# Kernel tuning notes

Hardware: AMD Instinct MI355X
Metric: run time of the kernel (lower is better)

Reference implementation:

```python
import jax, jax.numpy as jnp
import numpy as np

B, N, DI, DS, DP, DM, S = 64, 4096, 64, 64, 64, 128, 7
NUM_ITER = 3
EPS_ATTN = 1e-8
LN_EPS = 1e-5


def setup_inputs() -> dict:
    key = jax.random.key(0)
    ks = jax.random.split(key, 12)
    rn = lambda k, shp, sc=1.0: (jax.random.normal(k, shp, jnp.float32) * sc)
    return {
        "x": rn(ks[0], (B, N, DI)),
        "ln_inp_g": jnp.ones((DI,), jnp.float32),
        "ln_inp_b": jnp.zeros((DI,), jnp.float32),
        "ln_slot_g": jnp.ones((DS,), jnp.float32),
        "ln_slot_b": jnp.zeros((DS,), jnp.float32),
        "slots_init": rn(ks[1], (1, S, DS)),
        "Wk": rn(ks[2], (DI, DP), 1.0 / np.sqrt(DI)),
        "Wv": rn(ks[3], (DI, DP), 1.0 / np.sqrt(DI)),
        "Wq": rn(ks[4], (DS, DP), 1.0 / np.sqrt(DS)),
        "gru_wih": rn(ks[5], (3 * DS, DP), 1.0 / np.sqrt(DS)),
        "gru_whh": rn(ks[6], (3 * DS, DS), 1.0 / np.sqrt(DS)),
        "gru_bih": jnp.zeros((3 * DS,), jnp.float32),
        "gru_bhh": jnp.zeros((3 * DS,), jnp.float32),
        "mlp_w1": rn(ks[7], (DS, DM), 1.0 / np.sqrt(DS)),
        "mlp_b1": jnp.zeros((DM,), jnp.float32),
        "mlp_w2": rn(ks[8], (DM, DS), 1.0 / np.sqrt(DM)),
        "mlp_b2": jnp.zeros((DS,), jnp.float32),
    }


def _layernorm(x, g, b):
    m = jnp.mean(x, axis=-1, keepdims=True)
    v = jnp.mean(jnp.square(x - m), axis=-1, keepdims=True)
    return (x - m) * jax.lax.rsqrt(v + LN_EPS) * g + b


def _gru_cell(u, h, wih, whh, bih, bhh):
    # PyTorch GRUCell semantics
    gi = u @ wih.T + bih  # [*, 3*DS]
    gh = h @ whh.T + bhh
    ir, iz, inn = jnp.split(gi, 3, axis=-1)
    hr, hz, hn = jnp.split(gh, 3, axis=-1)
    r = jax.nn.sigmoid(ir + hr)
    z = jax.nn.sigmoid(iz + hz)
    n = jnp.tanh(inn + r * hn)
    return (1.0 - z) * n + z * h


def reference(x, ln_inp_g, ln_inp_b, ln_slot_g, ln_slot_b, slots_init,
              Wk, Wv, Wq, gru_wih, gru_whh, gru_bih, gru_bhh,
              mlp_w1, mlp_b1, mlp_w2, mlp_b2):
    x = _layernorm(x, ln_inp_g, ln_inp_b)          # [B,N,DI]
    k = x @ Wk                                      # [B,N,DP] (hoisted; x fixed across iters)
    v = x @ Wv                                      # [B,N,DP]
    slots = jnp.broadcast_to(slots_init, (x.shape[0], S, DS))
    scale = 1.0 / np.sqrt(DP)
    for _ in range(NUM_ITER):
        slots_prev = slots
        sn = _layernorm(slots, ln_slot_g, ln_slot_b)
        q = sn @ Wq                                 # [B,S,DP]
        attn = jnp.einsum('bnd,bsd->bns', k, q) * scale
        attn = jax.nn.softmax(attn, axis=-1) + EPS_ATTN      # softmax over slots
        weights = attn / jnp.sum(attn, axis=1, keepdims=True)  # normalize over N
        updates = jnp.einsum('bns,bnd->bsd', weights, v)     # [B,S,DP]
        h = _gru_cell(updates.reshape(-1, DP), slots_prev.reshape(-1, DS),
                      gru_wih, gru_whh, gru_bih, gru_bhh)
        slots = h.reshape(-1, S, DS)
        slots = slots + (jax.nn.relu(slots @ mlp_w1 + mlp_b1) @ mlp_w2 + mlp_b2)
    return slots
```

## Files before the change

### kernel.cpp

```cpp
#include <hip/hip_runtime.h>
#include <stdint.h>

#define L2E 1.44269504088896f

static __device__ __forceinline__ float wsum(float v) {
    #pragma unroll
    for (int m = 1; m < 64; m <<= 1) v += __shfl_xor(v, m, 64);
    return v;
}
static __device__ __forceinline__ float sigm(float x) {
    return 1.0f / (1.0f + __builtin_amdgcn_exp2f(-x * L2E));
}
static __device__ __forceinline__ float tanh_(float x) {
    const float ax = fabsf(x);
    const float t = __builtin_amdgcn_exp2f(-2.0f * ax * L2E);
    const float r = (1.0f - t) / (1.0f + t);
    return (x < 0.f) ? -r : r;
}

template <int CTRL>
static __device__ __forceinline__ float dppterm(float v) {
    return __int_as_float(__builtin_amdgcn_update_dpp(
        0, __float_as_int(v), CTRL, 0xF, 0xF, true));
}
static __device__ __forceinline__ float red8(float v) {
    v += dppterm<0xB1>(v);
    v += dppterm<0x4E>(v);
    v += dppterm<0x141>(v);
    return v;
}

__global__ __launch_bounds__(256) void init_kernel(
    const float* __restrict__ s0,
    const float* __restrict__ lsg, const float* __restrict__ lsb,
    const float* __restrict__ Wq,  const float* __restrict__ Wk,
    const float* __restrict__ lig, const float* __restrict__ lib,
    const float* __restrict__ wih, const float* __restrict__ whh,
    float* __restrict__ slots, float* __restrict__ gkq, float* __restrict__ aux,
    float* __restrict__ wihT, float* __restrict__ whhT, float* __restrict__ WkT)
{
    __shared__ float wkT[4096];
    __shared__ float scr[4][64];
    const int tid = threadIdx.x, lane = tid & 63, wv = tid >> 6;
    const int idx = blockIdx.x * 256 + tid;

    if (idx < 12288) {
        const int i = idx / 192, j = idx - i * 192;
        wihT[idx] = wih[j * 64 + i];
    } else if (idx < 24576) {
        const int o = idx - 12288;
        const int i = o / 192, j = o - i * 192;
        whhT[o] = whh[j * 64 + i];
    } else {
        const int o = idx - 24576;
        const int p = o >> 6, d = o & 63;
        WkT[o] = Wk[d * 64 + p];
    }

    const int r = blockIdx.x * 4 + wv;
    const int s = r % 7;
    #pragma unroll
    for (int i = tid; i < 4096; i += 256) {
        const int d = i >> 6, p = i & 63;
        wkT[p * 64 + d] = Wk[i];
    }
    const float h = s0[s * 64 + lane];
    slots[r * 64 + lane] = h;
    __syncthreads();

    const float mean = wsum(h) * (1.0f / 64.0f);
    const float d = h - mean;
    const float var = wsum(d * d) * (1.0f / 64.0f);
    const float rs = rsqrtf(var + 1e-5f);
    const float sn = d * rs * lsg[lane] + lsb[lane];
    scr[wv][lane] = sn;
    __syncthreads();
    float q = 0.f;
    #pragma unroll 8
    for (int i = 0; i < 64; ++i) q = fmaf(scr[wv][i], Wq[i * 64 + lane], q);
    q *= 0.125f;
    __syncthreads();
    scr[wv][lane] = q;
    __syncthreads();
    float kq = 0.f;
    #pragma unroll 8
    for (int p = 0; p < 64; ++p) kq = fmaf(wkT[p * 64 + lane], scr[wv][p], kq);
    const float bk = wsum(lib[lane] * kq);
    const float gk = lig[lane] * kq;
    const float g1 = wsum(gk);
    gkq[r * 64 + lane] = gk;
    if (lane == 0) { aux[r * 2] = g1; aux[r * 2 + 1] = bk; }
}

__global__ __launch_bounds__(256, 2) void attn_kernel(
    const float* __restrict__ x,
    const float* __restrict__ gkq, const float* __restrict__ aux,
    float* __restrict__ Ypart)
{
    __shared__ float ybuf[16][460];
    const int tid = threadIdx.x, lane = tid & 63, wv = tid >> 6;
    const int b = blockIdx.x >> 4, chunk16 = blockIdx.x & 15;
    const int ck  = lane & 7;
    const int rsl = lane >> 3;

    float gk[7][8];
    {
        const float4* gp = (const float4*)(gkq + b * 448 + ck * 8);
        #pragma unroll
        for (int s = 0; s < 7; ++s) {
            const float4 u0 = gp[s * 16], u1 = gp[s * 16 + 1];
            gk[s][0] = u0.x; gk[s][1] = u0.y; gk[s][2] = u0.z; gk[s][3] = u0.w;
            gk[s][4] = u1.x; gk[s][5] = u1.y; gk[s][6] = u1.z; gk[s][7] = u1.w;
        }
    }
    const float* ab = aux + b * 14;
    float g1[7], bk[7];
    #pragma unroll
    for (int s = 0; s < 7; ++s) { g1[s] = ab[2 * s]; bk[s] = ab[2 * s + 1]; }

    float Yacc[7][8];
    #pragma unroll
    for (int s = 0; s < 7; ++s)
        #pragma unroll
        for (int j = 0; j < 8; ++j) Yacc[s][j] = 0.f;
    float cacc[7] = {0.f, 0.f, 0.f, 0.f, 0.f, 0.f, 0.f};

    const float* rb = x + (((long)b * 4096) + chunk16 * 256 + wv * 64 + rsl) * 64
                        + ck * 8;
    float4 a0 = *(const float4*)(rb);
    float4 a1 = *(const float4*)(rb + 4);
    #pragma unroll 1
    for (int g = 0; g < 8; ++g) {
        const int gn = (g < 7) ? g + 1 : 7;
        const float4 b0 = *(const float4*)(rb + gn * 512);
        const float4 b1 = *(const float4*)(rb + gn * 512 + 4);

        const float xv[8] = {a0.x, a0.y, a0.z, a0.w, a1.x, a1.y, a1.z, a1.w};
        float sum = 0.f, ss = 0.f;
        #pragma unroll
        for (int j = 0; j < 8; ++j) { sum += xv[j]; ss = fmaf(xv[j], xv[j], ss); }
        float acc[7];
        #pragma unroll
        for (int s = 0; s < 7; ++s) {
            float a = 0.f;
            #pragma unroll
            for (int j = 0; j < 8; ++j) a = fmaf(xv[j], gk[s][j], a);
            acc[s] = a;
        }
        sum = red8(sum);
        ss  = red8(ss);
        #pragma unroll
        for (int s = 0; s < 7; ++s) acc[s] = red8(acc[s]);

        const float m   = sum * (1.0f / 64.0f);
        const float var = ss * (1.0f / 64.0f) - m * m;
        const float rs  = rsqrtf(var + 1e-5f);
        const float rsm = rs * m;
        float t[7];
        #pragma unroll
        for (int s = 0; s < 7; ++s)
            t[s] = fmaf(rs, acc[s], fmaf(-rsm, g1[s], bk[s]));
        float mx = t[0];
        #pragma unroll
        for (int s = 1; s < 7; ++s) mx = fmaxf(mx, t[s]);
        float e[7], se = 0.f;
        #pragma unroll
        for (int s = 0; s < 7; ++s) {
            e[s] = __builtin_amdgcn_exp2f((t[s] - mx) * L2E);
            se += e[s];
        }
        const float inv = 1.0f / se;
        #pragma unroll
        for (int s = 0; s < 7; ++s) {
            const float w = fmaf(e[s], inv, 1e-8f);
            cacc[s] += w;
            const float wrs = w * rs;
            #pragma unroll
            for (int j = 0; j < 8; ++j)
                Yacc[s][j] = fmaf(wrs, xv[j], Yacc[s][j]);
        }
        a0 = b0; a1 = b1;
    }

    #pragma unroll
    for (int s = 0; s < 7; ++s) {
        #pragma unroll
        for (int j = 0; j < 8; ++j)
            Yacc[s][j] += dppterm<0x128>(Yacc[s][j]);
        cacc[s] += dppterm<0x128>(cacc[s]);
    }
    if (((lane >> 3) & 1) == 0) {
        const int sub = lane >> 4;
        float* yb = &ybuf[wv * 4 + sub][ck * 8];
        #pragma unroll
        for (int s = 0; s < 7; ++s) {
            #pragma unroll
            for (int j = 0; j < 8; ++j) yb[s * 64 + j] = Yacc[s][j];
        }
        if (ck == 0) {
            #pragma unroll
            for (int s = 0; s < 7; ++s)
                ybuf[wv * 4 + sub][448 + s] = cacc[s];
        }
    }
    __syncthreads();
    for (int i = tid; i < 455; i += 256) {
        float v = 0.f;
        #pragma unroll
        for (int p = 0; p < 16; ++p) v += ybuf[p][i];
        Ypart[((long)b * 16 + chunk16) * 456 + i] = v;
    }
}

__global__ __launch_bounds__(512) void update_kernel(
    const float* __restrict__ Ypart, float* __restrict__ slots,
    const float* __restrict__ Wv,
    const float* __restrict__ wihT, const float* __restrict__ whhT,
    const float* __restrict__ bih,  const float* __restrict__ bhh,
    const float* __restrict__ w1,   const float* __restrict__ b1,
    const float* __restrict__ w2,   const float* __restrict__ b2,
    const float* __restrict__ lsg,  const float* __restrict__ lsb,
    const float* __restrict__ Wq,   const float* __restrict__ WkT,
    const float* __restrict__ lig,  const float* __restrict__ lib,
    float* __restrict__ gkq, float* __restrict__ aux,
    float* __restrict__ out, int last)
{
    __shared__ float wsYd[7][64];
    __shared__ float wsC[8];
    __shared__ float wss[7][4][64];
    const int tid = threadIdx.x, lane = tid & 63, wv = tid >> 6;
    const int b = blockIdx.x;
    const float* Yb = Ypart + (long)b * 16 * 456;

    if (tid < 448) {
        float v = 0.f;
        #pragma unroll
        for (int c = 0; c < 16; ++c) v += Yb[c * 456 + tid];
        wsYd[tid >> 6][tid & 63] = v;
    } else if (tid < 455) {
        const int s = tid - 448;
        float v = 0.f;
        #pragma unroll
        for (int c = 0; c < 16; ++c) v += Yb[c * 456 + 448 + s];
        wsC[s] = v;
    }
    __syncthreads();

    if (wv < 7) {
        const int s = wv;
        const int r = b * 7 + s;
        float (*scr)[64] = wss[wv];

        const float Yd = wsYd[s][lane];
        const float C  = wsC[s];
        const float Z  = wsum(Yd) * (1.0f / 64.0f);
        const float a  = (lig[lane] * (Yd - Z) + lib[lane] * C) / C;
        scr[0][lane] = a;
        float u = 0.f;
        #pragma unroll 8
        for (int i = 0; i < 64; ++i) u = fmaf(scr[0][i], Wv[i * 64 + lane], u);
        const float h = slots[r * 64 + lane];
        scr[1][lane] = u;
        scr[2][lane] = h;

        float gi0 = bih[lane], gi1 = bih[64 + lane], gi2 = bih[128 + lane];
        float gh0 = bhh[lane], gh1 = bhh[64 + lane], gh2 = bhh[128 + lane];
        #pragma unroll 4
        for (int i = 0; i < 64; ++i) {
            const float ui = scr[1][i], hi = scr[2][i];
            const float* wi = &wihT[i * 192];
            const float* wh = &whhT[i * 192];
            gi0 = fmaf(ui, wi[lane], gi0);
            gi1 = fmaf(ui, wi[64 + lane], gi1);
            gi2 = fmaf(ui, wi[128 + lane], gi2);
            gh0 = fmaf(hi, wh[lane], gh0);
            gh1 = fmaf(hi, wh[64 + lane], gh1);
            gh2 = fmaf(hi, wh[128 + lane], gh2);
        }
        const float rr = sigm(gi0 + gh0);
        const float zz = sigm(gi1 + gh1);
        const float nn = tanh_(gi2 + rr * gh2);
        const float hn = (1.f - zz) * nn + zz * h;
        scr[0][lane] = hn;

        float m0 = b1[lane], m1 = b1[64 + lane];
        #pragma unroll 8
        for (int i = 0; i < 64; ++i) {
            const float hi = scr[0][i];
            m0 = fmaf(hi, w1[i * 128 + lane], m0);
            m1 = fmaf(hi, w1[i * 128 + 64 + lane], m1);
        }
        scr[1][lane] = fmaxf(m0, 0.f);
        scr[2][lane] = fmaxf(m1, 0.f);

        float o2 = b2[lane];
        #pragma unroll 8
        for (int t = 0; t < 64; ++t)
            o2 = fmaf(scr[1][t], w2[t * 64 + lane], o2);
        #pragma unroll 8
        for (int t = 0; t < 64; ++t)
            o2 = fmaf(scr[2][t], w2[(64 + t) * 64 + lane], o2);
        const float snv = hn + o2;
        slots[r * 64 + lane] = snv;
        if (last) {
            out[r * 64 + lane] = snv;
        } else {
            const float mean = wsum(snv) * (1.0f / 64.0f);
            const float d = snv - mean;
            const float var = wsum(d * d) * (1.0f / 64.0f);
            const float rs = rsqrtf(var + 1e-5f);
            const float sn = d * rs * lsg[lane] + lsb[lane];
            scr[3][lane] = sn;
            float q = 0.f;
            #pragma unroll 8
            for (int i = 0; i < 64; ++i) q = fmaf(scr[3][i], Wq[i * 64 + lane], q);
            q *= 0.125f;
            scr[0][lane] = q;
            float kq = 0.f;
            #pragma unroll 8
            for (int p = 0; p < 64; ++p) kq = fmaf(WkT[p * 64 + lane], scr[0][p], kq);
            const float bk2 = wsum(lib[lane] * kq);
            const float gkv = lig[lane] * kq;
            const float g1v = wsum(gkv);
            gkq[r * 64 + lane] = gkv;
            if (lane == 0) { aux[r * 2] = g1v; aux[r * 2 + 1] = bk2; }
        }
    }
}

extern "C" void kernel_launch(void* const* d_in, const int* in_sizes, int n_in,
                              void* d_out, int out_size, void* d_ws, size_t ws_size,
                              hipStream_t stream)
{
    const float* x   = (const float*)d_in[0];
    const float* lig = (const float*)d_in[1];
    const float* lib = (const float*)d_in[2];
    const float* lsg = (const float*)d_in[3];
    const float* lsb = (const float*)d_in[4];
    const float* s0  = (const float*)d_in[5];
    const float* Wk  = (const float*)d_in[6];
    const float* Wv  = (const float*)d_in[7];
    const float* Wq  = (const float*)d_in[8];
    const float* wih = (const float*)d_in[9];
    const float* whh = (const float*)d_in[10];
    const float* bih = (const float*)d_in[11];
    const float* bhh = (const float*)d_in[12];
    const float* w1  = (const float*)d_in[13];
    const float* b1  = (const float*)d_in[14];
    const float* w2  = (const float*)d_in[15];
    const float* b2  = (const float*)d_in[16];

    float* f = (float*)d_ws;
    float* gkq   = f; f += 448 * 64;
    float* aux   = f; f += 448 * 2;
    float* slots = f; f += 448 * 64;
    float* Ypart = f; f += (long)64 * 16 * 456;
    float* wihT  = f; f += 64 * 192;
    float* whhT  = f; f += 64 * 192;
    float* WkT   = f; f += 64 * 64;

    init_kernel<<<112, 256, 0, stream>>>(s0, lsg, lsb, Wq, Wk, lig, lib,
                                         wih, whh, slots, gkq, aux,
                                         wihT, whhT, WkT);
    for (int it = 0; it < 3; ++it) {
        attn_kernel<<<1024, 256, 0, stream>>>(x, gkq, aux, Ypart);
        update_kernel<<<64, 512, 0, stream>>>(
            Ypart, slots, Wv, wihT, whhT, bih, bhh, w1, b1, w2, b2,
            lsg, lsb, Wq, WkT, lig, lib, gkq, aux,
            (float*)d_out, it == 2);
    }
}
```

Before: 240.4 us.

## Fuse slot update into attention blocks and cache per-row layernorm stats

```diff
diff --git a/kernel.cpp b/kernel.cpp
--- a/kernel.cpp
+++ b/kernel.cpp
@@ -92,10 +92,10 @@
     if (lane == 0) { aux[r * 2] = g1; aux[r * 2 + 1] = bk; }
 }
 
-__global__ __launch_bounds__(256, 2) void attn_kernel(
+__global__ __launch_bounds__(256, 2) void attn_first(
     const float* __restrict__ x,
     const float* __restrict__ gkq, const float* __restrict__ aux,
-    float* __restrict__ Ypart)
+    float* __restrict__ Ypart, float2* __restrict__ stats)
 {
     __shared__ float ybuf[16][460];
     const int tid = threadIdx.x, lane = tid & 63, wv = tid >> 6;
@@ -125,15 +125,15 @@
         for (int j = 0; j < 8; ++j) Yacc[s][j] = 0.f;
     float cacc[7] = {0.f, 0.f, 0.f, 0.f, 0.f, 0.f, 0.f};
 
-    const float* rb = x + (((long)b * 4096) + chunk16 * 256 + wv * 64 + rsl) * 64
-                        + ck * 8;
+    const int rowbase = chunk16 * 256 + wv * 64 + rsl;
+    const float* rb = x + ((long)b * 4096 + rowbase) * 64 + ck * 8;
     float4 a0 = *(const float4*)(rb);
     float4 a1 = *(const float4*)(rb + 4);
     #pragma unroll 1
     for (int g = 0; g < 8; ++g) {
         const int gn = (g < 7) ? g + 1 : 7;
-        const float4 b0 = *(const float4*)(rb + gn * 512);
-        const float4 b1 = *(const float4*)(rb + gn * 512 + 4);
+        const float4 n0 = *(const float4*)(rb + gn * 512);
+        const float4 n1 = *(const float4*)(rb + gn * 512 + 4);
 
         const float xv[8] = {a0.x, a0.y, a0.z, a0.w, a1.x, a1.y, a1.z, a1.w};
         float sum = 0.f, ss = 0.f;
@@ -155,6 +155,8 @@
         const float m   = sum * (1.0f / 64.0f);
         const float var = ss * (1.0f / 64.0f) - m * m;
         const float rs  = rsqrtf(var + 1e-5f);
+        if (ck == 0)
+            stats[(long)b * 4096 + rowbase + g * 8] = make_float2(m, rs);
         const float rsm = rs * m;
         float t[7];
         #pragma unroll
@@ -179,7 +181,7 @@
             for (int j = 0; j < 8; ++j)
                 Yacc[s][j] = fmaf(wrs, xv[j], Yacc[s][j]);
         }
-        a0 = b0; a1 = b1;
+        a0 = n0; a1 = n1;
     }
 
     #pragma unroll
@@ -212,8 +214,10 @@
     }
 }
 
-__global__ __launch_bounds__(512) void update_kernel(
-    const float* __restrict__ Ypart, float* __restrict__ slots,
+__global__ __launch_bounds__(256, 2) void attn_fused(
+    const float* __restrict__ x, const float2* __restrict__ stats,
+    const float* __restrict__ Yprev, float* __restrict__ Ycur,
+    const float* __restrict__ slots_rd, float* __restrict__ slots_wr,
     const float* __restrict__ Wv,
     const float* __restrict__ wihT, const float* __restrict__ whhT,
     const float* __restrict__ bih,  const float* __restrict__ bhh,
@@ -221,90 +225,100 @@
     const float* __restrict__ w2,   const float* __restrict__ b2,
     const float* __restrict__ lsg,  const float* __restrict__ lsb,
     const float* __restrict__ Wq,   const float* __restrict__ WkT,
-    const float* __restrict__ lig,  const float* __restrict__ lib,
-    float* __restrict__ gkq, float* __restrict__ aux,
-    float* __restrict__ out, int last)
+    const float* __restrict__ lig,  const float* __restrict__ lib)
 {
+    __shared__ float ybuf[16][460];
     __shared__ float wsYd[7][64];
     __shared__ float wsC[8];
-    __shared__ float wss[7][4][64];
+    __shared__ float wss[4][4][64];
+    __shared__ float gkql[448];
+    __shared__ float auxl[14];
     const int tid = threadIdx.x, lane = tid & 63, wv = tid >> 6;
-    const int b = blockIdx.x;
-    const float* Yb = Ypart + (long)b * 16 * 456;
-
-    if (tid < 448) {
+    const int b = blockIdx.x >> 4, chunk16 = blockIdx.x & 15;
+    const int ck  = lane & 7;
+    const int rsl = lane >> 3;
+
+    const int rowbase = chunk16 * 256 + wv * 64 + rsl;
+    const float* rb = x + ((long)b * 4096 + rowbase) * 64 + ck * 8;
+    float4 a0 = *(const float4*)(rb);
+    float4 a1 = *(const float4*)(rb + 4);
+    float2 st = stats[(long)b * 4096 + rowbase];
+
+    const float* Yb = Yprev + (long)b * 16 * 456;
+    for (int o = tid; o < 448; o += 256) {
         float v = 0.f;
         #pragma unroll
-        for (int c = 0; c < 16; ++c) v += Yb[c * 456 + tid];
-        wsYd[tid >> 6][tid & 63] = v;
-    } else if (tid < 455) {
-        const int s = tid - 448;
+        for (int c = 0; c < 16; ++c) v += Yb[c * 456 + o];
+        wsYd[o >> 6][o & 63] = v;
+    }
+    if (tid < 7) {
         float v = 0.f;
         #pragma unroll
-        for (int c = 0; c < 16; ++c) v += Yb[c * 456 + 448 + s];
-        wsC[s] = v;
-    }
-    __syncthreads();
-
-    if (wv < 7) {
-        const int s = wv;
-        const int r = b * 7 + s;
+        for (int c = 0; c < 16; ++c) v += Yb[c * 456 + 448 + tid];
+        wsC[tid] = v;
+    }
+    __syncthreads();
+
+    {
         float (*scr)[64] = wss[wv];
-
-        const float Yd = wsYd[s][lane];
-        const float C  = wsC[s];
-        const float Z  = wsum(Yd) * (1.0f / 64.0f);
-        const float a  = (lig[lane] * (Yd - Z) + lib[lane] * C) / C;
-        scr[0][lane] = a;
-        float u = 0.f;
-        #pragma unroll 8
-        for (int i = 0; i < 64; ++i) u = fmaf(scr[0][i], Wv[i * 64 + lane], u);
-        const float h = slots[r * 64 + lane];
-        scr[1][lane] = u;
-        scr[2][lane] = h;
-
-        float gi0 = bih[lane], gi1 = bih[64 + lane], gi2 = bih[128 + lane];
-        float gh0 = bhh[lane], gh1 = bhh[64 + lane], gh2 = bhh[128 + lane];
-        #pragma unroll 4
-        for (int i = 0; i < 64; ++i) {
-            const float ui = scr[1][i], hi = scr[2][i];
-            const float* wi = &wihT[i * 192];
-            const float* wh = &whhT[i * 192];
-            gi0 = fmaf(ui, wi[lane], gi0);
-            gi1 = fmaf(ui, wi[64 + lane], gi1);
-            gi2 = fmaf(ui, wi[128 + lane], gi2);
-            gh0 = fmaf(hi, wh[lane], gh0);
-            gh1 = fmaf(hi, wh[64 + lane], gh1);
-            gh2 = fmaf(hi, wh[128 + lane], gh2);
-        }
-        const float rr = sigm(gi0 + gh0);
-        const float zz = sigm(gi1 + gh1);
-        const float nn = tanh_(gi2 + rr * gh2);
-        const float hn = (1.f - zz) * nn + zz * h;
-        scr[0][lane] = hn;
-
-        float m0 = b1[lane], m1 = b1[64 + lane];
-        #pragma unroll 8
-        for (int i = 0; i < 64; ++i) {
-            const float hi = scr[0][i];
-            m0 = fmaf(hi, w1[i * 128 + lane], m0);
-            m1 = fmaf(hi, w1[i * 128 + 64 + lane], m1);
-        }
-        scr[1][lane] = fmaxf(m0, 0.f);
-        scr[2][lane] = fmaxf(m1, 0.f);
-
-        float o2 = b2[lane];
-        #pragma unroll 8
-        for (int t = 0; t < 64; ++t)
-            o2 = fmaf(scr[1][t], w2[t * 64 + lane], o2);
-        #pragma unroll 8
-        for (int t = 0; t < 64; ++t)
-            o2 = fmaf(scr[2][t], w2[(64 + t) * 64 + lane], o2);
-        const float snv = hn + o2;
-        slots[r * 64 + lane] = snv;
-        if (last) {
-            out[r * 64 + lane] = snv;
-        } else {
+        #pragma unroll 1
+        for (int sp = 0; sp < 2; ++sp) {
+            const int s = wv + sp * 4;
+            if (s >= 7) break;
+            const int r = b * 7 + s;
+
+            const float Yd = wsYd[s][lane];
+            const float C  = wsC[s];
+            const float Z  = wsum(Yd) * (1.0f / 64.0f);
+            const float a  = (lig[lane] * (Yd - Z) + lib[lane] * C) / C;
+            scr[0][lane] = a;
+            float u = 0.f;
+            #pragma unroll 8
+            for (int i = 0; i < 64; ++i) u = fmaf(scr[0][i], Wv[i * 64 + lane], u);
+            const float h = slots_rd[r * 64 + lane];
+            scr[1][lane] = u;
+            scr[2][lane] = h;
+
+            float gi0 = bih[lane], gi1 = bih[64 + lane], gi2 = bih[128 + lane];
+            float gh0 = bhh[lane], gh1 = bhh[64 + lane], gh2 = bhh[128 + lane];
+            #pragma unroll 4
+            for (int i = 0; i < 64; ++i) {
+                const float ui = scr[1][i], hi = scr[2][i];
+                const float* wi = &wihT[i * 192];
+                const float* wh = &whhT[i * 192];
+                gi0 = fmaf(ui, wi[lane], gi0);
+                gi1 = fmaf(ui, wi[64 + lane], gi1);
+                gi2 = fmaf(ui, wi[128 + lane], gi2);
+                gh0 = fmaf(hi, wh[lane], gh0);
+                gh1 = fmaf(hi, wh[64 + lane], gh1);
+                gh2 = fmaf(hi, wh[128 + lane], gh2);
+            }
+            const float rr = sigm(gi0 + gh0);
+            const float zz = sigm(gi1 + gh1);
+            const float nn = tanh_(gi2 + rr * gh2);
+            const float hn = (1.f - zz) * nn + zz * h;
+            scr[0][lane] = hn;
+
+            float m0 = b1[lane], m1 = b1[64 + lane];
+            #pragma unroll 8
+            for (int i = 0; i < 64; ++i) {
+                const float hi = scr[0][i];
+                m0 = fmaf(hi, w1[i * 128 + lane], m0);
+                m1 = fmaf(hi, w1[i * 128 + 64 + lane], m1);
+            }
+            scr[1][lane] = fmaxf(m0, 0.f);
+            scr[2][lane] = fmaxf(m1, 0.f);
+
+            float o2 = b2[lane];
+            #pragma unroll 8
+            for (int t2 = 0; t2 < 64; ++t2)
+                o2 = fmaf(scr[1][t2], w2[t2 * 64 + lane], o2);
+            #pragma unroll 8
+            for (int t2 = 0; t2 < 64; ++t2)
+                o2 = fmaf(scr[2][t2], w2[(64 + t2) * 64 + lane], o2);
+            const float snv = hn + o2;
+            slots_wr[r * 64 + lane] = snv;
+
             const float mean = wsum(snv) * (1.0f / 64.0f);
             const float d = snv - mean;
             const float var = wsum(d * d) * (1.0f / 64.0f);
@@ -322,9 +336,193 @@
             const float bk2 = wsum(lib[lane] * kq);
             const float gkv = lig[lane] * kq;
             const float g1v = wsum(gkv);
-            gkq[r * 64 + lane] = gkv;
-            if (lane == 0) { aux[r * 2] = g1v; aux[r * 2 + 1] = bk2; }
-        }
+            gkql[s * 64 + lane] = gkv;
+            if (lane == 0) { auxl[2 * s] = g1v; auxl[2 * s + 1] = bk2; }
+        }
+    }
+    __syncthreads();
+
+    float gk[7][8];
+    #pragma unroll
+    for (int s = 0; s < 7; ++s) {
+        #pragma unroll
+        for (int j = 0; j < 8; ++j) gk[s][j] = gkql[s * 64 + ck * 8 + j];
+    }
+    float g1[7], bk[7];
+    #pragma unroll
+    for (int s = 0; s < 7; ++s) { g1[s] = auxl[2 * s]; bk[s] = auxl[2 * s + 1]; }
+
+    float Yacc[7][8];
+    #pragma unroll
+    for (int s = 0; s < 7; ++s)
+        #pragma unroll
+        for (int j = 0; j < 8; ++j) Yacc[s][j] = 0.f;
+    float cacc[7] = {0.f, 0.f, 0.f, 0.f, 0.f, 0.f, 0.f};
+
+    #pragma unroll 1
+    for (int g = 0; g < 8; ++g) {
+        const int gn = (g < 7) ? g + 1 : 7;
+        const float4 n0 = *(const float4*)(rb + gn * 512);
+        const float4 n1 = *(const float4*)(rb + gn * 512 + 4);
+        const float2 stn = stats[(long)b * 4096 + rowbase + gn * 8];
+
+        const float xv[8] = {a0.x, a0.y, a0.z, a0.w, a1.x, a1.y, a1.z, a1.w};
+        float acc[7];
+        #pragma unroll
+        for (int s = 0; s < 7; ++s) {
+            float a = 0.f;
+            #pragma unroll
+            for (int j = 0; j < 8; ++j) a = fmaf(xv[j], gk[s][j], a);
+            acc[s] = a;
+        }
+        #pragma unroll
+        for (int s = 0; s < 7; ++s) acc[s] = red8(acc[s]);
+
+        const float m  = st.x;
+        const float rs = st.y;
+        const float rsm = rs * m;
+        float t[7];
+        #pragma unroll
+        for (int s = 0; s < 7; ++s)
+            t[s] = fmaf(rs, acc[s], fmaf(-rsm, g1[s], bk[s]));
+        float mx = t[0];
+        #pragma unroll
+        for (int s = 1; s < 7; ++s) mx = fmaxf(mx, t[s]);
+        float e[7], se = 0.f;
+        #pragma unroll
+        for (int s = 0; s < 7; ++s) {
+            e[s] = __builtin_amdgcn_exp2f((t[s] - mx) * L2E);
+            se += e[s];
+        }
+        const float inv = 1.0f / se;
+        #pragma unroll
+        for (int s = 0; s < 7; ++s) {
+            const float w = fmaf(e[s], inv, 1e-8f);
+            cacc[s] += w;
+            const float wrs = w * rs;
+            #pragma unroll
+            for (int j = 0; j < 8; ++j)
+                Yacc[s][j] = fmaf(wrs, xv[j], Yacc[s][j]);
+        }
+        a0 = n0; a1 = n1; st = stn;
+    }
+
+    #pragma unroll
+    for (int s = 0; s < 7; ++s) {
+        #pragma unroll
+        for (int j = 0; j < 8; ++j)
+            Yacc[s][j] += dppterm<0x128>(Yacc[s][j]);
+        cacc[s] += dppterm<0x128>(cacc[s]);
+    }
+    if (((lane >> 3) & 1) == 0) {
+        const int sub = lane >> 4;
+        float* yb = &ybuf[wv * 4 + sub][ck * 8];
+        #pragma unroll
+        for (int s = 0; s < 7; ++s) {
+            #pragma unroll
+            for (int j = 0; j < 8; ++j) yb[s * 64 + j] = Yacc[s][j];
+        }
+        if (ck == 0) {
+            #pragma unroll
+            for (int s = 0; s < 7; ++s)
+                ybuf[wv * 4 + sub][448 + s] = cacc[s];
+        }
+    }
+    __syncthreads();
+    for (int i = tid; i < 455; i += 256) {
+        float v = 0.f;
+        #pragma unroll
+        for (int p = 0; p < 16; ++p) v += ybuf[p][i];
+        Ycur[((long)b * 16 + chunk16) * 456 + i] = v;
+    }
+}
+
+__global__ __launch_bounds__(512) void update_kernel(
+    const float* __restrict__ Ypart, float* __restrict__ slots,
+    const float* __restrict__ Wv,
+    const float* __restrict__ wihT, const float* __restrict__ whhT,
+    const float* __restrict__ bih,  const float* __restrict__ bhh,
+    const float* __restrict__ w1,   const float* __restrict__ b1,
+    const float* __restrict__ w2,   const float* __restrict__ b2,
+    const float* __restrict__ lig,  const float* __restrict__ lib,
+    float* __restrict__ out)
+{
+    __shared__ float wsYd[7][64];
+    __shared__ float wsC[8];
+    __shared__ float wss[7][4][64];
+    const int tid = threadIdx.x, lane = tid & 63, wv = tid >> 6;
+    const int b = blockIdx.x;
+    const float* Yb = Ypart + (long)b * 16 * 456;
+
+    if (tid < 448) {
+        float v = 0.f;
+        #pragma unroll
+        for (int c = 0; c < 16; ++c) v += Yb[c * 456 + tid];
+        wsYd[tid >> 6][tid & 63] = v;
+    } else if (tid < 455) {
+        const int s = tid - 448;
+        float v = 0.f;
+        #pragma unroll
+        for (int c = 0; c < 16; ++c) v += Yb[c * 456 + 448 + s];
+        wsC[s] = v;
+    }
+    __syncthreads();
+
+    if (wv < 7) {
+        const int s = wv;
+        const int r = b * 7 + s;
+        float (*scr)[64] = wss[wv];
+
+        const float Yd = wsYd[s][lane];
+        const float C  = wsC[s];
+        const float Z  = wsum(Yd) * (1.0f / 64.0f);
+        const float a  = (lig[lane] * (Yd - Z) + lib[lane] * C) / C;
+        scr[0][lane] = a;
+        float u = 0.f;
+        #pragma unroll 8
+        for (int i = 0; i < 64; ++i) u = fmaf(scr[0][i], Wv[i * 64 + lane], u);
+        const float h = slots[r * 64 + lane];
+        scr[1][lane] = u;
+        scr[2][lane] = h;
+
+        float gi0 = bih[lane], gi1 = bih[64 + lane], gi2 = bih[128 + lane];
+        float gh0 = bhh[lane], gh1 = bhh[64 + lane], gh2 = bhh[128 + lane];
+        #pragma unroll 4
+        for (int i = 0; i < 64; ++i) {
+            const float ui = scr[1][i], hi = scr[2][i];
+            const float* wi = &wihT[i * 192];
+            const float* wh = &whhT[i * 192];
+            gi0 = fmaf(ui, wi[lane], gi0);
+            gi1 = fmaf(ui, wi[64 + lane], gi1);
+            gi2 = fmaf(ui, wi[128 + lane], gi2);
+            gh0 = fmaf(hi, wh[lane], gh0);
+            gh1 = fmaf(hi, wh[64 + lane], gh1);
+            gh2 = fmaf(hi, wh[128 + lane], gh2);
+        }
+        const float rr = sigm(gi0 + gh0);
+        const float zz = sigm(gi1 + gh1);
+        const float nn = tanh_(gi2 + rr * gh2);
+        const float hn = (1.f - zz) * nn + zz * h;
+        scr[0][lane] = hn;
+
+        float m0 = b1[lane], m1 = b1[64 + lane];
+        #pragma unroll 8
+        for (int i = 0; i < 64; ++i) {
+            const float hi = scr[0][i];
+            m0 = fmaf(hi, w1[i * 128 + lane], m0);
+            m1 = fmaf(hi, w1[i * 128 + 64 + lane], m1);
+        }
+        scr[1][lane] = fmaxf(m0, 0.f);
+        scr[2][lane] = fmaxf(m1, 0.f);
+
+        float o2 = b2[lane];
+        #pragma unroll 8
+        for (int t = 0; t < 64; ++t)
+            o2 = fmaf(scr[1][t], w2[t * 64 + lane], o2);
+        #pragma unroll 8
+        for (int t = 0; t < 64; ++t)
+            o2 = fmaf(scr[2][t], w2[(64 + t) * 64 + lane], o2);
+        out[r * 64 + lane] = hn + o2;
     }
 }
 
@@ -353,20 +551,26 @@
     float* f = (float*)d_ws;
     float* gkq   = f; f += 448 * 64;
     float* aux   = f; f += 448 * 2;
-    float* slots = f; f += 448 * 64;
-    float* Ypart = f; f += (long)64 * 16 * 456;
+    float* sl0   = f; f += 448 * 64;
+    float* sl1   = f; f += 448 * 64;
+    float* Yp0   = f; f += (long)64 * 16 * 456;
+    float* Yp1   = f; f += (long)64 * 16 * 456;
     float* wihT  = f; f += 64 * 192;
     float* whhT  = f; f += 64 * 192;
     float* WkT   = f; f += 64 * 64;
+    float2* stats = (float2*)f; f += (long)2 * 64 * 4096;
 
     init_kernel<<<112, 256, 0, stream>>>(s0, lsg, lsb, Wq, Wk, lig, lib,
-                                         wih, whh, slots, gkq, aux,
+                                         wih, whh, sl0, gkq, aux,
                                          wihT, whhT, WkT);
-    for (int it = 0; it < 3; ++it) {
-        attn_kernel<<<1024, 256, 0, stream>>>(x, gkq, aux, Ypart);
-        update_kernel<<<64, 512, 0, stream>>>(
-            Ypart, slots, Wv, wihT, whhT, bih, bhh, w1, b1, w2, b2,
-            lsg, lsb, Wq, WkT, lig, lib, gkq, aux,
-            (float*)d_out, it == 2);
-    }
-}
+    attn_first<<<1024, 256, 0, stream>>>(x, gkq, aux, Yp0, stats);
+    attn_fused<<<1024, 256, 0, stream>>>(x, stats, Yp0, Yp1, sl0, sl1,
+                                         Wv, wihT, whhT, bih, bhh, w1, b1,
+                                         w2, b2, lsg, lsb, Wq, WkT, lig, lib);
+    attn_fused<<<1024, 256, 0, stream>>>(x, stats, Yp1, Yp0, sl1, sl0,
+                                         Wv, wihT, whhT, bih, bhh, w1, b1,
+                                         w2, b2, lsg, lsb, Wq, WkT, lig, lib);
+    update_kernel<<<64, 512, 0, stream>>>(Yp0, sl0, Wv, wihT, whhT, bih, bhh,
+                                          w1, b1, w2, b2, lig, lib,
+                                          (float*)d_out);
+}
```

Measured after the change: 315.7 us. 31.3% more time.
